# Performance work log

Hardware: AMD Instinct MI355X
Metric: run time of the kernel (lower is better)

The kernel has to match this reference:

```python
import jax, jax.numpy as jnp
import numpy as np

N_FFT = 1024
HOP = 256
N_MELS = 80
SR = 16000
N_ITER = 32
MOMENTUM = 0.99
B, T = 8, 1024


def _mel_filterbank(sr, n_fft, n_mels):
    # librosa.filters.mel (htk=False, norm='slaney') reimplemented in numpy
    f_sp = 200.0 / 3
    min_log_hz = 1000.0
    min_log_mel = min_log_hz / f_sp
    logstep = np.log(6.4) / 27.0

    def hz_to_mel(f):
        f = np.asarray(f, dtype=np.float64)
        return np.where(f >= min_log_hz,
                        min_log_mel + np.log(np.maximum(f, 1e-10) / min_log_hz) / logstep,
                        f / f_sp)

    def mel_to_hz(m):
        m = np.asarray(m, dtype=np.float64)
        return np.where(m >= min_log_mel,
                        min_log_hz * np.exp(logstep * (m - min_log_mel)),
                        m * f_sp)

    fftfreqs = np.linspace(0.0, sr / 2.0, n_fft // 2 + 1)
    mel_f = mel_to_hz(np.linspace(hz_to_mel(0.0), hz_to_mel(sr / 2.0), n_mels + 2))
    fdiff = np.diff(mel_f)
    ramps = mel_f[:, None] - fftfreqs[None, :]
    lower = -ramps[:-2] / fdiff[:-1][:, None]
    upper = ramps[2:] / fdiff[1:][:, None]
    weights = np.maximum(0.0, np.minimum(lower, upper))
    enorm = 2.0 / (mel_f[2:n_mels + 2] - mel_f[:n_mels])  # slaney norm
    return (weights * enorm[:, None]).astype(np.float32)


def _hann(n):
    return (0.5 - 0.5 * jnp.cos(2.0 * jnp.pi * jnp.arange(n) / n)).astype(jnp.float32)


def _stft(x, window):
    # x: [B, L] real -> [B, n_fft//2+1, F] complex (center=True, reflect pad)
    pad = N_FFT // 2
    xp = jnp.pad(x, ((0, 0), (pad, pad)), mode='reflect')
    n_frames = 1 + (xp.shape[-1] - N_FFT) // HOP
    idx = jnp.arange(n_frames)[:, None] * HOP + jnp.arange(N_FFT)[None, :]
    frames = xp[:, idx] * window  # [B, F, n_fft]
    return jnp.fft.rfft(frames, axis=-1).transpose(0, 2, 1)


def _istft(S, window):
    # S: [B, n_fft//2+1, F] complex -> [B, hop*(F-1)] real (center=True)
    bsz, _, n_frames = S.shape
    frames = jnp.fft.irfft(S.transpose(0, 2, 1), n=N_FFT, axis=-1) * window  # [B,F,n_fft]
    out_len = N_FFT + HOP * (n_frames - 1)
    idx = (jnp.arange(n_frames)[:, None] * HOP + jnp.arange(N_FFT)[None, :]).ravel()
    y = jnp.zeros((bsz, out_len), frames.dtype).at[:, idx].add(frames.reshape(bsz, -1))
    wsq = jnp.zeros((out_len,), window.dtype).at[idx].add(jnp.tile(window ** 2, n_frames))
    y = y / jnp.maximum(wsq, 1e-8)
    pad = N_FFT // 2
    return y[:, pad:-pad]


def _griffin_lim(mag, angles0, window):
    # mag: [B, bins, F] real magnitude, angles0 in [0,1)
    Sc = mag.astype(jnp.complex64)
    angles = jnp.exp(2j * jnp.pi * angles0).astype(jnp.complex64)
    rebuilt = jnp.zeros_like(Sc)
    beta = MOMENTUM / (1.0 + MOMENTUM)

    def body(carry, _):
        ang, reb_prev = carry
        inv = _istft(Sc * ang, window)
        reb = _stft(inv, window)
        new_ang = reb - beta * reb_prev
        new_ang = new_ang / (jnp.abs(new_ang) + 1e-16)
        return (new_ang, reb), None

    (angles, _), _ = jax.lax.scan(body, (angles, rebuilt), None, length=N_ITER)
    return _istft(Sc * angles, window)


def setup_inputs() -> dict:
    key = jax.random.key(0)
    k1, k2 = jax.random.split(key)
    mel_spec = jax.random.normal(k1, (B, N_MELS, T), dtype=jnp.float32)
    mel_basis = _mel_filterbank(SR, N_FFT, N_MELS)          # [80, 513]
    mel_inverse = jnp.asarray(np.linalg.pinv(mel_basis))     # [513, 80]
    angles0 = jax.random.uniform(k2, (B, N_FFT // 2 + 1, T), dtype=jnp.float32)
    return {"mel_spec": mel_spec, "mel_inverse": mel_inverse, "angles0": angles0}


def reference(mel_spec, mel_inverse, angles0):
    window = _hann(N_FFT)
    # mel -> linear magnitude spectrogram; |spec * e^{i theta}| == |spec|
    spec = jnp.einsum('fm,bmt->bft', mel_inverse, jnp.exp(mel_spec))
    mag = jnp.abs(spec)
    audio = _griffin_lim(mag, angles0, window)  # [B, hop*(T-1)]
    return audio
```

## Files before the change

### kernel.cpp

```cpp
#include <hip/hip_runtime.h>
#include <math.h>

#define BATCH    8
#define NFFT     1024
#define HOPSZ    256
#define NBINS    513
#define SROW     516
#define TFRAMES  1024
#define NBLK     (BATCH * TFRAMES)
#define LOUT     261888
#define YLEN     262912
#define NITER    32

#define LDSIDX(i) ((i) + ((i) >> 5))
#define LDSBUF    532

__device__ __forceinline__ void wsync() {
    __asm__ volatile("s_waitcnt lgkmcnt(0)" ::: "memory");
}

template <int SIGN>
__device__ __forceinline__ void dft8(const float xr[8], const float xi[8],
                                     float yr[8], float yi[8])
{
    const float r2 = 0.70710678118654752f;
    float Ar = xr[0] + xr[4], Ai = xi[0] + xi[4];
    float Br = xr[0] - xr[4], Bi = xi[0] - xi[4];
    float Cr = xr[2] + xr[6], Ci = xi[2] + xi[6];
    float Dr = xr[2] - xr[6], Di = xi[2] - xi[6];
    float E0r = Ar + Cr, E0i = Ai + Ci;
    float E2r = Ar - Cr, E2i = Ai - Ci;
    float E1r, E1i, E3r, E3i;
    if (SIGN < 0) { E1r = Br + Di; E1i = Bi - Dr; E3r = Br - Di; E3i = Bi + Dr; }
    else          { E1r = Br - Di; E1i = Bi + Dr; E3r = Br + Di; E3i = Bi - Dr; }
    float ar = xr[1] + xr[5], ai = xi[1] + xi[5];
    float br = xr[1] - xr[5], bi = xi[1] - xi[5];
    float cr = xr[3] + xr[7], ci = xi[3] + xi[7];
    float dr = xr[3] - xr[7], di = xi[3] - xi[7];
    float O0r = ar + cr, O0i = ai + ci;
    float O2r = ar - cr, O2i = ai - ci;
    float O1r, O1i, O3r, O3i;
    if (SIGN < 0) { O1r = br + di; O1i = bi - dr; O3r = br - di; O3i = bi + dr; }
    else          { O1r = br - di; O1i = bi + dr; O3r = br + di; O3i = bi - dr; }
    float t1r, t1i, t2r, t2i, t3r, t3i;
    if (SIGN < 0) {
        t1r = r2 * (O1r + O1i); t1i = r2 * (O1i - O1r);
        t2r = O2i;              t2i = -O2r;
        t3r = r2 * (O3i - O3r); t3i = -r2 * (O3r + O3i);
    } else {
        t1r = r2 * (O1r - O1i); t1i = r2 * (O1i + O1r);
        t2r = -O2i;             t2i = O2r;
        t3r = -r2 * (O3r + O3i); t3i = r2 * (O3r - O3i);
    }
    yr[0] = E0r + O0r; yi[0] = E0i + O0i;  yr[4] = E0r - O0r; yi[4] = E0i - O0i;
    yr[1] = E1r + t1r; yi[1] = E1i + t1i;  yr[5] = E1r - t1r; yi[5] = E1i - t1i;
    yr[2] = E2r + t2r; yi[2] = E2i + t2i;  yr[6] = E2r - t2r; yi[6] = E2i - t2i;
    yr[3] = E3r + t3r; yi[3] = E3i + t3i;  yr[7] = E3r - t3r; yi[7] = E3i - t3i;
}

template <int SIGN, int S>
__device__ __forceinline__ void stage_write(float* lre, float* lim,
                                            const float yr[8], const float yi[8],
                                            int lane, const float2* __restrict__ tw)
{
    const int q = lane & (S - 1);
    const int p = lane / S;
    const int e = p * S;
    const int base = q + 8 * S * p;
#pragma unroll
    for (int j = 0; j < 8; ++j) {
        float vr = yr[j], vi = yi[j];
        if (j > 0) {
            float2 w = tw[j * e];
            float wr = w.x, wi = (SIGN < 0) ? w.y : -w.y;
            float tr = vr * wr - vi * wi;
            vi = vr * wi + vi * wr;
            vr = tr;
        }
        int o = LDSIDX(base + S * j);
        lre[o] = vr; lim[o] = vi;
    }
}

__device__ __forceinline__ void stage_read(const float* lre, const float* lim,
                                           float xr[8], float xi[8], int lane)
{
#pragma unroll
    for (int j = 0; j < 8; ++j) {
        int o = LDSIDX(lane + 64 * j);
        xr[j] = lre[o]; xi[j] = lim[o];
    }
}

template <int SIGN>
__device__ __forceinline__ void fft512(float* lre, float* lim,
                                       float xr[8], float xi[8],
                                       float yr[8], float yi[8],
                                       int lane, const float2* __restrict__ tw)
{
    dft8<SIGN>(xr, xi, yr, yi);
    stage_write<SIGN, 1>(lre, lim, yr, yi, lane, tw);
    wsync();
    stage_read(lre, lim, xr, xi, lane);
    wsync();
    dft8<SIGN>(xr, xi, yr, yi);
    stage_write<SIGN, 8>(lre, lim, yr, yi, lane, tw);
    wsync();
    stage_read(lre, lim, xr, xi, lane);
    dft8<SIGN>(xr, xi, yr, yi);
}

template <int SIGN>
__device__ __forceinline__ void fft512_lds(float* lre, float* lim,
                                           float xr[8], float xi[8],
                                           float yr[8], float yi[8],
                                           int lane, const float2* __restrict__ tw)
{
    stage_read(lre, lim, xr, xi, lane);
    wsync();
    fft512<SIGN>(lre, lim, xr, xi, yr, yi, lane, tw);
}

__global__ void k_tables(float2* tw512, float2* twh, float* win, float* wscl)
{
    int i = blockIdx.x * blockDim.x + threadIdx.x;
    if (i < 512) {
        double t1 = -2.0 * M_PI * (double)i / 512.0;
        tw512[i] = make_float2((float)cos(t1), (float)sin(t1));
        double t2 = -2.0 * M_PI * (double)i / 1024.0;
        twh[i] = make_float2((float)cos(t2), (float)sin(t2));
    }
    if (i < 1024) {
        double w = 0.5 - 0.5 * cos(2.0 * M_PI * (double)i / 1024.0);
        win[i]  = (float)w;
        wscl[i] = (float)(w / 512.0);
    }
}

__global__ void k_wsq(const float* __restrict__ win, float* __restrict__ wsqinv)
{
    int t = blockIdx.x * blockDim.x + threadIdx.x;
    if (t >= YLEN) return;
    int fhi = t >> 8;
    int flo = fhi - 3; if (flo < 0) flo = 0;
    if (fhi > TFRAMES - 1) fhi = TFRAMES - 1;
    float acc = 0.f;
    for (int f = flo; f <= fhi; ++f) {
        float w = win[t - (f << 8)];
        acc += w * w;
    }
    float m = acc > 1e-8f ? acc : 1e-8f;
    wsqinv[t] = 1.0f / m;
}

__global__ void k_melinvT(const float* __restrict__ melinv, float* __restrict__ melinvT)
{
    int idx = blockIdx.x * blockDim.x + threadIdx.x;
    if (idx >= 80 * NBINS) return;
    int m = idx / NBINS, k = idx - m * NBINS;
    melinvT[idx] = melinv[k * 80 + m];
}

__global__ __launch_bounds__(256) void k_angT(const float* __restrict__ ang0,
                                              float* __restrict__ angT)
{
    __shared__ float tile[32][33];
    int kt = blockIdx.x * 32, tt = blockIdx.y * 32, b = blockIdx.z;
    int tx = threadIdx.x & 31, ty = threadIdx.x >> 5;
#pragma unroll
    for (int i = 0; i < 32; i += 8) {
        int k = kt + ty + i, t = tt + tx;
        if (k < NBINS) tile[ty + i][tx] = ang0[((size_t)b * NBINS + k) * 1024 + t];
    }
    __syncthreads();
#pragma unroll
    for (int i = 0; i < 32; i += 8) {
        int t = tt + ty + i, k = kt + tx;
        if (k < NBINS) angT[((size_t)b * 1024 + t) * NBINS + k] = tile[tx][ty + i];
    }
}

__global__ __launch_bounds__(256) void k_specinit(const float* __restrict__ mel,
                                                  const float* __restrict__ melinvT,
                                                  const float* __restrict__ angT,
                                                  float* __restrict__ mag,
                                                  float2* __restrict__ spec)
{
    int blk = blockIdx.x;
    int b = blk >> 10;
    int t = blk & 1023;
    int tid = threadIdx.x;
    __shared__ float em[80];
    if (tid < 80) em[tid] = expf(mel[((size_t)b * 80 + tid) * 1024 + t]);
    __syncthreads();
    size_t row = (size_t)blk * SROW;
    size_t arow = ((size_t)b * 1024 + t) * NBINS;
    for (int k = tid; k < NBINS; k += 256) {
        float s = 0.f;
#pragma unroll 8
        for (int m = 0; m < 80; ++m) s += melinvT[m * NBINS + k] * em[m];
        float mg = fabsf(s);
        float a = angT[arow + k];
        float sn, cn;
        sincospif(2.0f * a, &sn, &cn);
        mag[row + k] = mg;
        spec[row + k] = make_float2(mg * cn, mg * sn);
    }
}

__global__ __launch_bounds__(256) void k_ifft(const float2* __restrict__ spec,
                                              const float2* __restrict__ tw512,
                                              const float2* __restrict__ twh,
                                              const float* __restrict__ wscl,
                                              float* __restrict__ frames)
{
    __shared__ float scr[4][2][LDSBUF];
    int tid = threadIdx.x;
    int w = tid >> 6, lane = tid & 63;
    int blk = blockIdx.x * 4 + w;
    size_t row = (size_t)blk * SROW;
    float* lre = scr[w][0];
    float* lim = scr[w][1];

    float xr[8], xi[8], yr[8], yi[8];
#pragma unroll
    for (int r = 0; r < 8; ++r) {
        int k = lane + 64 * r;
        float2 v1 = spec[row + k];
        float2 v2 = spec[row + 512 - k];
        if (k == 0) { v1.y = 0.f; v2.y = 0.f; }
        float Ar = 0.5f * (v1.x + v2.x), Ai = 0.5f * (v1.y - v2.y);
        float Sr = 0.5f * (v1.x - v2.x), Si = 0.5f * (v1.y + v2.y);
        float2 W = twh[k];
        float Xor = W.x * Sr + W.y * Si;
        float Xoi = W.x * Si - W.y * Sr;
        xr[r] = Ar - Xoi;
        xi[r] = Ai + Xor;
    }
    fft512<1>(lre, lim, xr, xi, yr, yi, lane, tw512);
    size_t frow = (size_t)blk * 1024;
#pragma unroll
    for (int j = 0; j < 8; ++j) {
        int m = lane + 64 * j;
        float2 ws = *(const float2*)&wscl[2 * m];
        float2 o;
        o.x = yr[j] * ws.x;
        o.y = yi[j] * ws.y;
        *(float2*)&frames[frow + 2 * m] = o;
    }
}

__global__ __launch_bounds__(256) void k_oa(const float* __restrict__ frames,
                                            const float* __restrict__ wsqinv,
                                            float* __restrict__ audioR)
{
    int t = blockIdx.x * 256 + threadIdx.x;
    int b = blockIdx.y;
    const float* fb = frames + (size_t)b * (TFRAMES * 1024);
    int fhi = t >> 8;
    int flo = fhi - 3; if (flo < 0) flo = 0;
    if (fhi > TFRAMES - 1) fhi = TFRAMES - 1;
    float acc = 0.f;
    for (int ff = flo; ff <= fhi; ++ff)
        acc += fb[(size_t)ff * 1024 + (t - (ff << 8))];
    audioR[(size_t)b * YLEN + t] = acc * wsqinv[t];
}

__global__ __launch_bounds__(256) void k_fused(const float* __restrict__ audioR,
                                               const float* __restrict__ mag,
                                               const float2* __restrict__ tw512,
                                               const float2* __restrict__ twh,
                                               const float* __restrict__ win,
                                               const float* __restrict__ wscl,
                                               float2* __restrict__ rebprev,
                                               float* __restrict__ frames,
                                               float beta)
{
    __shared__ float scr[4][2][LDSBUF];
    int tid = threadIdx.x;
    int w = tid >> 6, lane = tid & 63;
    int blk = blockIdx.x * 4 + w;
    int b = blk >> 10;
    int f = blk & 1023;
    const float* ab = audioR + (size_t)b * YLEN;
    float* lre = scr[w][0];
    float* lim = scr[w][1];

    float xr[8], xi[8], yr[8], yi[8];
    if (f >= 2 && f <= 1021) {
        const float* src = ab + f * HOPSZ;
#pragma unroll
        for (int j = 0; j < 8; ++j) {
            int n0 = 2 * (lane + 64 * j);
            float2 s = *(const float2*)&src[n0];
            float2 w2 = *(const float2*)&win[n0];
            xr[j] = s.x * w2.x;
            xi[j] = s.y * w2.y;
        }
    } else {
#pragma unroll
        for (int j = 0; j < 8; ++j) {
            int n0 = 2 * (lane + 64 * j);
            int j0 = f * HOPSZ + n0 - 512;
            int ja = (j0 < 0) ? -j0 : ((j0 >= LOUT) ? 2 * LOUT - 2 - j0 : j0);
            int j1 = j0 + 1;
            int jb = (j1 < 0) ? -j1 : ((j1 >= LOUT) ? 2 * LOUT - 2 - j1 : j1);
            float s0 = ab[ja + 512];
            float s1 = ab[jb + 512];
            float2 w2 = *(const float2*)&win[n0];
            xr[j] = s0 * w2.x;
            xi[j] = s1 * w2.y;
        }
    }
    fft512<-1>(lre, lim, xr, xi, yr, yi, lane, tw512);

#pragma unroll
    for (int j = 0; j < 8; ++j) {
        int o = LDSIDX(lane + 64 * j);
        lre[o] = yr[j]; lim[o] = yi[j];
    }
    wsync();

    size_t row = (size_t)blk * SROW;
#pragma unroll
    for (int r = 0; r < 5; ++r) {
        int p;
        if (r < 4) p = lane + 64 * r;
        else { if (lane != 0) break; p = 256; }
        int pm = (512 - p) & 511;
        float Zkr = lre[LDSIDX(p)],  Zki = lim[LDSIDX(p)];
        float Zmr = lre[LDSIDX(pm)], Zmi = lim[LDSIDX(pm)];
        float Ar = 0.5f * (Zkr + Zmr), Ai = 0.5f * (Zki - Zmi);
        float Sr = 0.5f * (Zkr - Zmr), Si = 0.5f * (Zki + Zmi);
        float2 W1 = twh[p];
        float U1r = W1.x * Sr - W1.y * Si, U1i = W1.x * Si + W1.y * Sr;
        float Xpr = Ar + U1i, Xpi = Ai - U1r;
        float w2r, w2i;
        if (p == 0) { w2r = -1.f; w2i = 0.f; }
        else { float2 W2 = twh[512 - p]; w2r = W2.x; w2i = W2.y; }
        float U2r = -w2r * Sr - w2i * Si, U2i = w2r * Si - w2i * Sr;
        float Xqr = Ar + U2i, Xqi = -Ai - U2r;
        int q = 512 - p;
        float2 pv1 = rebprev[row + p];
        float2 pv2 = rebprev[row + q];
        float v1x = Xpr - beta * pv1.x, v1y = Xpi - beta * pv1.y;
        float v2x = Xqr - beta * pv2.x, v2y = Xqi - beta * pv2.y;
        float a1 = sqrtf(v1x * v1x + v1y * v1y) + 1e-16f;
        float a2 = sqrtf(v2x * v2x + v2y * v2y) + 1e-16f;
        float sc1 = mag[row + p] / a1;
        float sc2 = mag[row + q] / a2;
        float s1x = v1x * sc1, s1y = v1y * sc1;
        float s2x = v2x * sc2, s2y = v2y * sc2;
        rebprev[row + p] = make_float2(Xpr, Xpi);
        rebprev[row + q] = make_float2(Xqr, Xqi);
        float Apr = 0.5f * (s1x + s2x), Api = 0.5f * (s1y - s2y);
        float Spr = 0.5f * (s1x - s2x), Spi = 0.5f * (s1y + s2y);
        float Xor = W1.x * Spr + W1.y * Spi;
        float Xoi = W1.x * Spi - W1.y * Spr;
        lre[LDSIDX(p)] = Apr - Xoi;
        lim[LDSIDX(p)] = Api + Xor;
        if (p > 0) {
            float Yor = -w2r * Spr + w2i * Spi;
            float Yoi = w2r * Spi + w2i * Spr;
            lre[LDSIDX(512 - p)] = Apr - Yoi;
            lim[LDSIDX(512 - p)] = -Api + Yor;
        }
    }
    wsync();

    fft512_lds<1>(lre, lim, xr, xi, yr, yi, lane, tw512);
    size_t frow = (size_t)blk * 1024;
#pragma unroll
    for (int j = 0; j < 8; ++j) {
        int m = lane + 64 * j;
        float2 ws = *(const float2*)&wscl[2 * m];
        float2 o;
        o.x = yr[j] * ws.x;
        o.y = yi[j] * ws.y;
        *(float2*)&frames[frow + 2 * m] = o;
    }
}

__global__ __launch_bounds__(256) void k_gather(const float* __restrict__ frames,
                                                const float* __restrict__ wsqinv,
                                                float* __restrict__ out)
{
    int idx = blockIdx.x * 256 + threadIdx.x;
    if (idx >= BATCH * LOUT) return;
    int b = idx / LOUT;
    int j = idx - b * LOUT;
    int t = j + 512;
    const float* fb = frames + (size_t)b * (TFRAMES * 1024);
    int fhi = t >> 8;
    int flo = fhi - 3; if (flo < 0) flo = 0;
    if (fhi > TFRAMES - 1) fhi = TFRAMES - 1;
    float acc = 0.f;
    for (int ff = flo; ff <= fhi; ++ff)
        acc += fb[(size_t)ff * 1024 + (t - (ff << 8))];
    out[idx] = acc * wsqinv[t];
}

extern "C" void kernel_launch(void* const* d_in, const int* in_sizes, int n_in,
                              void* d_out, int out_size, void* d_ws, size_t ws_size,
                              hipStream_t stream)
{
    const float* mel    = (const float*)d_in[0];
    const float* melinv = (const float*)d_in[1];
    const float* ang0   = (const float*)d_in[2];
    float* out = (float*)d_out;

    char* ws = (char*)d_ws;
    size_t off = 0;
    auto carve = [&](size_t bytes) -> void* {
        void* p = ws + off;
        off += (bytes + 255) & ~(size_t)255;
        return p;
    };
    float2* tw512   = (float2*)carve(512 * sizeof(float2));
    float2* twh     = (float2*)carve(512 * sizeof(float2));
    float*  win     = (float*) carve(1024 * sizeof(float));
    float*  wscl    = (float*) carve(1024 * sizeof(float));
    float*  wsqinv  = (float*) carve((size_t)YLEN * sizeof(float));
    float*  melinvT = (float*) carve((size_t)80 * NBINS * sizeof(float));
    float*  mag     = (float*) carve((size_t)NBLK * SROW * sizeof(float));
    float2* spec    = (float2*)carve((size_t)NBLK * SROW * sizeof(float2));
    float2* rebp    = (float2*)carve((size_t)NBLK * SROW * sizeof(float2));
    float*  frames  = (float*) carve((size_t)NBLK * 1024 * sizeof(float));
    float*  audioR  = (float*) carve((size_t)BATCH * YLEN * sizeof(float));
    float*  angT    = frames;
    (void)ws_size; (void)in_sizes; (void)n_in; (void)out_size;

    const float beta = (float)(0.99 / 1.99);

    hipLaunchKernelGGL(k_tables, dim3(4), dim3(256), 0, stream, tw512, twh, win, wscl);
    hipLaunchKernelGGL(k_wsq, dim3((YLEN + 255) / 256), dim3(256), 0, stream, win, wsqinv);
    hipLaunchKernelGGL(k_melinvT, dim3((80 * NBINS + 255) / 256), dim3(256), 0, stream,
                       melinv, melinvT);
    hipLaunchKernelGGL(k_angT, dim3(17, 32, BATCH), dim3(256), 0, stream, ang0, angT);
    hipLaunchKernelGGL(k_specinit, dim3(NBLK), dim3(256), 0, stream,
                       mel, melinvT, angT, mag, spec);
    (void)hipMemsetAsync(rebp, 0, (size_t)NBLK * SROW * sizeof(float2), stream);

    hipLaunchKernelGGL(k_ifft, dim3(NBLK / 4), dim3(256), 0, stream,
                       spec, tw512, twh, wscl, frames);
    for (int it = 0; it < NITER; ++it) {
        hipLaunchKernelGGL(k_oa, dim3(YLEN / 256, BATCH), dim3(256), 0, stream,
                           frames, wsqinv, audioR);
        hipLaunchKernelGGL(k_fused, dim3(NBLK / 4), dim3(256), 0, stream,
                           audioR, mag, tw512, twh, win, wscl, rebp, frames, beta);
    }
    hipLaunchKernelGGL(k_gather, dim3((BATCH * LOUT + 255) / 256), dim3(256), 0, stream,
                       frames, wsqinv, out);
}
```

Baseline: 1.398 ms.

## Fuse overlap-add into STFT kernel with ping-pong frame buffers

Removes the separate overlap-add kernel per iteration: the fused STFT kernel now reconstructs each audio sample directly from up to four overlapping iSTFT frames, and frame buffers alternate between a dedicated buffer and the reused spec buffer. Setup kernels are merged into one launch. This cuts one launch and one audio-buffer write/read per iteration but makes each sample read roughly 4 frame values (redundant global reads, mostly cache-served) instead of one.

```diff
diff --git a/kernel.cpp b/kernel.cpp
--- a/kernel.cpp
+++ b/kernel.cpp
@@ -121,44 +121,40 @@
     fft512<SIGN>(lre, lim, xr, xi, yr, yi, lane, tw);
 }
 
-__global__ void k_tables(float2* tw512, float2* twh, float* win, float* wscl)
-{
-    int i = blockIdx.x * blockDim.x + threadIdx.x;
-    if (i < 512) {
-        double t1 = -2.0 * M_PI * (double)i / 512.0;
-        tw512[i] = make_float2((float)cos(t1), (float)sin(t1));
-        double t2 = -2.0 * M_PI * (double)i / 1024.0;
-        twh[i] = make_float2((float)cos(t2), (float)sin(t2));
-    }
-    if (i < 1024) {
-        double w = 0.5 - 0.5 * cos(2.0 * M_PI * (double)i / 1024.0);
-        win[i]  = (float)w;
-        wscl[i] = (float)(w / 512.0);
-    }
-}
-
-__global__ void k_wsq(const float* __restrict__ win, float* __restrict__ wsqinv)
-{
-    int t = blockIdx.x * blockDim.x + threadIdx.x;
-    if (t >= YLEN) return;
-    int fhi = t >> 8;
-    int flo = fhi - 3; if (flo < 0) flo = 0;
-    if (fhi > TFRAMES - 1) fhi = TFRAMES - 1;
-    float acc = 0.f;
-    for (int f = flo; f <= fhi; ++f) {
-        float w = win[t - (f << 8)];
-        acc += w * w;
-    }
-    float m = acc > 1e-8f ? acc : 1e-8f;
-    wsqinv[t] = 1.0f / m;
-}
-
-__global__ void k_melinvT(const float* __restrict__ melinv, float* __restrict__ melinvT)
+__global__ void k_setup(float2* tw512, float2* twh, float* win, float* wscl,
+                        const float* __restrict__ melinv, float* __restrict__ melinvT,
+                        float* __restrict__ wsqinv)
 {
     int idx = blockIdx.x * blockDim.x + threadIdx.x;
-    if (idx >= 80 * NBINS) return;
-    int m = idx / NBINS, k = idx - m * NBINS;
-    melinvT[idx] = melinv[k * 80 + m];
+    if (idx < 512) {
+        double t1 = -2.0 * M_PI * (double)idx / 512.0;
+        tw512[idx] = make_float2((float)cos(t1), (float)sin(t1));
+        double t2 = -2.0 * M_PI * (double)idx / 1024.0;
+        twh[idx] = make_float2((float)cos(t2), (float)sin(t2));
+    }
+    if (idx < 1024) {
+        double w = 0.5 - 0.5 * cos(2.0 * M_PI * (double)idx / 1024.0);
+        win[idx]  = (float)w;
+        wscl[idx] = (float)(w / 512.0);
+    }
+    if (idx < 80 * NBINS) {
+        int m = idx / NBINS, k = idx - m * NBINS;
+        melinvT[idx] = melinv[k * 80 + m];
+    }
+    if (idx < YLEN) {
+        int t = idx;
+        int fhi = t >> 8;
+        int flo = fhi - 3; if (flo < 0) flo = 0;
+        if (fhi > TFRAMES - 1) fhi = TFRAMES - 1;
+        float acc = 0.f;
+        for (int f = flo; f <= fhi; ++f) {
+            int n = t - (f << 8);
+            float w = (float)(0.5 - 0.5 * cos(2.0 * M_PI * (double)n / 1024.0));
+            acc += w * w;
+        }
+        float m = acc > 1e-8f ? acc : 1e-8f;
+        wsqinv[t] = 1.0f / m;
+    }
 }
 
 __global__ __launch_bounds__(256) void k_angT(const float* __restrict__ ang0,
@@ -221,7 +217,6 @@
     size_t row = (size_t)blk * SROW;
     float* lre = scr[w][0];
     float* lim = scr[w][1];
-
     float xr[8], xi[8], yr[8], yi[8];
 #pragma unroll
     for (int r = 0; r < 8; ++r) {
@@ -250,30 +245,27 @@
     }
 }
 
-__global__ __launch_bounds__(256) void k_oa(const float* __restrict__ frames,
-                                            const float* __restrict__ wsqinv,
-                                            float* __restrict__ audioR)
-{
-    int t = blockIdx.x * 256 + threadIdx.x;
-    int b = blockIdx.y;
-    const float* fb = frames + (size_t)b * (TFRAMES * 1024);
+__device__ __forceinline__ float oa_sample(const float* __restrict__ fb, int t,
+                                           const float* __restrict__ wsqinv)
+{
     int fhi = t >> 8;
     int flo = fhi - 3; if (flo < 0) flo = 0;
     if (fhi > TFRAMES - 1) fhi = TFRAMES - 1;
     float acc = 0.f;
     for (int ff = flo; ff <= fhi; ++ff)
         acc += fb[(size_t)ff * 1024 + (t - (ff << 8))];
-    audioR[(size_t)b * YLEN + t] = acc * wsqinv[t];
-}
-
-__global__ __launch_bounds__(256) void k_fused(const float* __restrict__ audioR,
+    return acc * wsqinv[t];
+}
+
+__global__ __launch_bounds__(256) void k_fused(const float* __restrict__ framesIn,
                                                const float* __restrict__ mag,
                                                const float2* __restrict__ tw512,
                                                const float2* __restrict__ twh,
                                                const float* __restrict__ win,
                                                const float* __restrict__ wscl,
+                                               const float* __restrict__ wsqinv,
                                                float2* __restrict__ rebprev,
-                                               float* __restrict__ frames,
+                                               float* __restrict__ framesOut,
                                                float beta)
 {
     __shared__ float scr[4][2][LDSBUF];
@@ -282,20 +274,21 @@
     int blk = blockIdx.x * 4 + w;
     int b = blk >> 10;
     int f = blk & 1023;
-    const float* ab = audioR + (size_t)b * YLEN;
+    const float* fb = framesIn + (size_t)b * (TFRAMES * 1024);
     float* lre = scr[w][0];
     float* lim = scr[w][1];
 
     float xr[8], xi[8], yr[8], yi[8];
     if (f >= 2 && f <= 1021) {
-        const float* src = ab + f * HOPSZ;
 #pragma unroll
         for (int j = 0; j < 8; ++j) {
             int n0 = 2 * (lane + 64 * j);
-            float2 s = *(const float2*)&src[n0];
+            int t0 = f * HOPSZ + n0;
+            float s0 = oa_sample(fb, t0, wsqinv);
+            float s1 = oa_sample(fb, t0 + 1, wsqinv);
             float2 w2 = *(const float2*)&win[n0];
-            xr[j] = s.x * w2.x;
-            xi[j] = s.y * w2.y;
+            xr[j] = s0 * w2.x;
+            xi[j] = s1 * w2.y;
         }
     } else {
 #pragma unroll
@@ -305,8 +298,8 @@
             int ja = (j0 < 0) ? -j0 : ((j0 >= LOUT) ? 2 * LOUT - 2 - j0 : j0);
             int j1 = j0 + 1;
             int jb = (j1 < 0) ? -j1 : ((j1 >= LOUT) ? 2 * LOUT - 2 - j1 : j1);
-            float s0 = ab[ja + 512];
-            float s1 = ab[jb + 512];
+            float s0 = oa_sample(fb, ja + 512, wsqinv);
+            float s1 = oa_sample(fb, jb + 512, wsqinv);
             float2 w2 = *(const float2*)&win[n0];
             xr[j] = s0 * w2.x;
             xi[j] = s1 * w2.y;
@@ -361,7 +354,7 @@
         lim[LDSIDX(p)] = Api + Xor;
         if (p > 0) {
             float Yor = -w2r * Spr + w2i * Spi;
-            float Yoi = w2r * Spi + w2i * Spr;
+            float Yoi =  w2r * Spi + w2i * Spr;
             lre[LDSIDX(512 - p)] = Apr - Yoi;
             lim[LDSIDX(512 - p)] = -Api + Yor;
         }
@@ -377,7 +370,7 @@
         float2 o;
         o.x = yr[j] * ws.x;
         o.y = yi[j] * ws.y;
-        *(float2*)&frames[frow + 2 * m] = o;
+        *(float2*)&framesOut[frow + 2 * m] = o;
     }
 }
 
@@ -389,15 +382,8 @@
     if (idx >= BATCH * LOUT) return;
     int b = idx / LOUT;
     int j = idx - b * LOUT;
-    int t = j + 512;
     const float* fb = frames + (size_t)b * (TFRAMES * 1024);
-    int fhi = t >> 8;
-    int flo = fhi - 3; if (flo < 0) flo = 0;
-    if (fhi > TFRAMES - 1) fhi = TFRAMES - 1;
-    float acc = 0.f;
-    for (int ff = flo; ff <= fhi; ++ff)
-        acc += fb[(size_t)ff * 1024 + (t - (ff << 8))];
-    out[idx] = acc * wsqinv[t];
+    out[idx] = oa_sample(fb, j + 512, wsqinv);
 }
 
 extern "C" void kernel_launch(void* const* d_in, const int* in_sizes, int n_in,
@@ -425,30 +411,28 @@
     float*  mag     = (float*) carve((size_t)NBLK * SROW * sizeof(float));
     float2* spec    = (float2*)carve((size_t)NBLK * SROW * sizeof(float2));
     float2* rebp    = (float2*)carve((size_t)NBLK * SROW * sizeof(float2));
-    float*  frames  = (float*) carve((size_t)NBLK * 1024 * sizeof(float));
-    float*  audioR  = (float*) carve((size_t)BATCH * YLEN * sizeof(float));
-    float*  angT    = frames;
+    float*  frames0 = (float*) carve((size_t)NBLK * 1024 * sizeof(float));
+    float* frames1 = (float*)spec;
+    float* angT    = frames0;
     (void)ws_size; (void)in_sizes; (void)n_in; (void)out_size;
 
     const float beta = (float)(0.99 / 1.99);
 
-    hipLaunchKernelGGL(k_tables, dim3(4), dim3(256), 0, stream, tw512, twh, win, wscl);
-    hipLaunchKernelGGL(k_wsq, dim3((YLEN + 255) / 256), dim3(256), 0, stream, win, wsqinv);
-    hipLaunchKernelGGL(k_melinvT, dim3((80 * NBINS + 255) / 256), dim3(256), 0, stream,
-                       melinv, melinvT);
+    hipLaunchKernelGGL(k_setup, dim3((YLEN + 255) / 256), dim3(256), 0, stream,
+                       tw512, twh, win, wscl, melinv, melinvT, wsqinv);
     hipLaunchKernelGGL(k_angT, dim3(17, 32, BATCH), dim3(256), 0, stream, ang0, angT);
     hipLaunchKernelGGL(k_specinit, dim3(NBLK), dim3(256), 0, stream,
                        mel, melinvT, angT, mag, spec);
     (void)hipMemsetAsync(rebp, 0, (size_t)NBLK * SROW * sizeof(float2), stream);
 
     hipLaunchKernelGGL(k_ifft, dim3(NBLK / 4), dim3(256), 0, stream,
-                       spec, tw512, twh, wscl, frames);
+                       spec, tw512, twh, wscl, frames0);
     for (int it = 0; it < NITER; ++it) {
-        hipLaunchKernelGGL(k_oa, dim3(YLEN / 256, BATCH), dim3(256), 0, stream,
-                           frames, wsqinv, audioR);
+        const float* fin = (it & 1) ? frames1 : frames0;
+        float*       fot = (it & 1) ? frames0 : frames1;
         hipLaunchKernelGGL(k_fused, dim3(NBLK / 4), dim3(256), 0, stream,
-                           audioR, mag, tw512, twh, win, wscl, rebp, frames, beta);
+                           fin, mag, tw512, twh, win, wscl, wsqinv, rebp, fot, beta);
     }
     hipLaunchKernelGGL(k_gather, dim3((BATCH * LOUT + 255) / 256), dim3(256), 0, stream,
-                       frames, wsqinv, out);
-}
+                       frames0, wsqinv, out);
+}
```

Result: slower. 1.775 ms (+27.0%).
